# Performance work log

Measured on AMD Instinct MI355X. Metric: run time of the kernel, lower is better.

Reference implementation:

```python
import jax, jax.numpy as jnp
import numpy as np

N = 100000   # nodes
C = 128      # in_channels
K = 32       # n_super_nodes
B = 16       # graphs in batch
TAU = 1.0
EPS = 1e-9
SPARSITY_W = 0.01
TEMPORAL_W = 0.1 * 5
COLLAPSE_W = 2.0


def setup_inputs() -> dict:
    key = jax.random.key(0)
    ks = jax.random.split(key, 8)
    x = jax.random.normal(ks[0], (N, C), dtype=jnp.float32)
    batch = jnp.sort(jax.random.randint(ks[1], (N,), 0, B)).astype(jnp.int64)
    pos = jax.random.normal(ks[2], (N, 2), dtype=jnp.float32)
    gumbel_u = jax.random.uniform(ks[3], (N, K), dtype=jnp.float32,
                                  minval=1e-6, maxval=1.0 - 1e-6)
    W1 = jax.random.normal(ks[4], (C, C), dtype=jnp.float32) / np.float32(np.sqrt(C))
    b1 = jnp.zeros((C,), jnp.float32)
    W2 = jax.random.normal(ks[5], (C, K), dtype=jnp.float32) / np.float32(np.sqrt(C))
    b2 = jnp.zeros((K,), jnp.float32)
    scaling = jnp.asarray(10.0, jnp.float32)
    active_mask = jnp.ones((K,), jnp.float32)
    return dict(x=x, batch=batch, pos=pos, gumbel_u=gumbel_u,
                W1=W1, b1=b1, W2=W2, b2=b2, scaling=scaling,
                active_mask=active_mask)


def reference(x, batch, pos, gumbel_u, W1, b1, W2, b2, scaling, active_mask):
    # assign MLP: Linear -> ReLU -> Linear, scaled
    h = jax.nn.relu(x @ W1 + b1)                      # [N, C]
    logits = (h @ W2 + b2) * scaling                  # [N, K]
    # eval-mode masking of inactive super-nodes (active_mask is a detached buffer)
    mask = jax.lax.stop_gradient(active_mask)[None, :]
    logits = jnp.where(mask == 0, -1e9, logits)
    # Gumbel-softmax (soft, hard=False) with explicit uniform noise
    g = -jnp.log(-jnp.log(gumbel_u + EPS) + EPS)
    s = jax.nn.softmax((logits + g) / TAU, axis=-1)   # [N, K]

    avg_s = s.mean(axis=0)                            # [K]
    entropy = -jnp.mean(jnp.sum(s * jnp.log(s + EPS), axis=1))
    uniform_p = 1.0 / K
    diversity = jnp.sum(uniform_p * jnp.log(uniform_p / (avg_s + EPS)))
    pruning = jnp.mean(jnp.abs(avg_s * (1.0 - active_mask)))
    sparsity = (jnp.sum(active_mask) / K) * SPARSITY_W
    temporal = jnp.asarray(0.0, s.dtype)  # prev_assignments=None

    # collapse prevention (common_losses approximation: normalized entropy
    # deficit + peak-mass penalty), scaled by collapse weight
    ent_avg = -jnp.sum(avg_s * jnp.log(avg_s + EPS))
    collapse = ((jnp.log(jnp.asarray(K, s.dtype)) - ent_avg)
                / jnp.log(jnp.asarray(K, s.dtype))
                + jax.nn.relu(jnp.max(avg_s) - 2.0 / K)) * COLLAPSE_W
    # balance (KL(avg_s || uniform))
    balance = jnp.sum(avg_s * jnp.log(avg_s * K + EPS))

    # spatial variance loss over column-normalized assignments
    s_sum = s.sum(axis=0, keepdims=True) + EPS        # [1, K]
    s_norm = s / s_sum                                # [N, K]
    mu = s_norm.T @ pos                               # [K, 2]
    pos_sq = jnp.sum(pos ** 2, axis=1, keepdims=True) # [N, 1]
    st_pos = s_norm.T @ pos                           # [K, 2]
    var = (s_norm.T @ pos_sq)[:, 0] - 2.0 * jnp.sum(mu * st_pos, axis=1) \
          + jnp.sum(mu ** 2, axis=1)
    spatial = var.mean()

    # per-graph super-node centroids via segment pooling
    sum_s_pos = jax.ops.segment_sum(pos[:, None, :] * s[:, :, None], batch,
                                    num_segments=B)   # [B, K, 2]
    sum_s = jax.ops.segment_sum(s, batch, num_segments=B)[:, :, None] + EPS
    super_node_mu = sum_s_pos / sum_s                 # [B, K, 2]

    # separation loss among centroids
    d = super_node_mu[:, :, None, :] - super_node_mu[:, None, :, :]
    dist_sq = jnp.sum(d ** 2, axis=-1)                # [B, K, K]
    eye = jnp.eye(K, dtype=s.dtype)[None]
    repulsion = 1.0 / (dist_sq + 1.0)
    separation = jnp.sum(repulsion * (1.0 - eye)) / (K * (K - 1) + EPS)

    # hierarchical pooling: out[b,k,c] = sum_{i in graph b} s[i,k] * x[i,c]
    x_expanded = x[:, None, :] * s[:, :, None]        # [N, K, C]
    out = jax.ops.segment_sum(x_expanded, batch, num_segments=B)  # [B, K, C]

    losses = jnp.stack([entropy, diversity, spatial, pruning, sparsity,
                        temporal * TEMPORAL_W, collapse, balance, separation])
    return out, s, super_node_mu, losses
```

## Files before the change

### kernel.cpp

```cpp
#include <hip/hip_runtime.h>
#include <math.h>

#define NN 100000
#define CC 128
#define KK 32
#define BG 16
#define EPSF 1e-9f

#define NTILES 1563

#define S_OFF 65536
#define MU_OFF 3265536
#define LOSS_OFF 3266560

#define WS_ENTARR 0
#define WS_STAT 2048
#define WS_FIRST 4096
#define WS_LAST 4112
#define WS_ZERO_FLOATS 4096

#define W1B_OFF_BYTES 16896
#define W2B_OFF_BYTES 49664
#define WS_PART_FLOAT 16384
#define WS_NEEDED_BYTES (65536ull + (unsigned long long)NTILES * 4096ull * 4ull)

typedef __attribute__((ext_vector_type(8))) _Float16 half8;
typedef __attribute__((ext_vector_type(4))) _Float16 half4v;
typedef __attribute__((ext_vector_type(4))) float float4v;

#define MFMAH(a, b, c) __builtin_amdgcn_mfma_f32_16x16x32_f16((a), (b), (c), 0, 0, 0)

__global__ __launch_bounds__(256) void k_prep(const float* __restrict__ W1,
                                              const float* __restrict__ W2,
                                              _Float16* __restrict__ wW1,
                                              _Float16* __restrict__ wW2,
                                              int* __restrict__ firstp,
                                              int* __restrict__ lastp) {
    int tid = blockIdx.x * 256 + threadIdx.x;
    if (tid < 8 * 4 * 64) {
        int l = tid & 63, ks = (tid >> 6) & 3, nt = tid >> 8;
        int n = nt * 16 + (l & 15);
        int cb = ks * 32 + (l >> 4) * 8;
        half8 H;
#pragma unroll
        for (int j = 0; j < 8; ++j) H[j] = (_Float16)W1[(size_t)(cb + j) * CC + n];
        ((half8*)wW1)[(nt * 4 + ks) * 64 + l] = H;
    } else if (tid < 2048 + 512) {
        int t2 = tid - 2048;
        int l = t2 & 63, ks = (t2 >> 6) & 3, nt = t2 >> 8;
        int n = nt * 16 + (l & 15);
        int cb = ks * 32 + (l >> 4) * 8;
        half8 H;
#pragma unroll
        for (int j = 0; j < 8; ++j) H[j] = (_Float16)W2[(size_t)(cb + j) * KK + n];
        ((half8*)wW2)[(nt * 4 + ks) * 64 + l] = H;
    } else if (tid < 2560 + 16) {
        firstp[tid - 2560] = 0x7fffffff;
    } else if (tid < 2576 + 16) {
        lastp[tid - 2576] = -1;
    }
}

__global__ __launch_bounds__(256, 4) void k_assign(
    const float* __restrict__ x, const int* __restrict__ batch,
    const float* __restrict__ pos, const float* __restrict__ gum,
    const float* __restrict__ b1, const float* __restrict__ b2,
    const float* __restrict__ scaling, const float* __restrict__ amask,
    const _Float16* __restrict__ wW1, const _Float16* __restrict__ wW2,
    float* __restrict__ dout, float* __restrict__ ws,
    float* __restrict__ part, int* __restrict__ firstp, int* __restrict__ lastp)
{
    __shared__ _Float16 xh[64][136];
    __shared__ _Float16 st[32][72];
    __shared__ float lpx[64], lpy[64], lpsq[64];
    __shared__ int lbat[64];
    float* sbuf = (float*)&xh[0][0];

    const int t = threadIdx.x;
    const bool usep = (part != nullptr);
    const int orig = blockIdx.x;
    const int qq = NTILES >> 3, rr8 = NTILES & 7;
    const int xcd = orig & 7, sidx = orig >> 3;
    const int tile = (xcd < rr8 ? xcd * (qq + 1) : rr8 * (qq + 1) + (xcd - rr8) * qq) + sidx;
    const int n0 = tile * 64;

    const int l = t & 63;
    const int wv = __builtin_amdgcn_readfirstlane(t >> 6);
    const int li = l & 15;
    const int g16 = l >> 4;
    const int cc4 = (t & 31) * 4;
    const int nb = t >> 5;
    const int ca  = (2 * wv) * 16 + li;
    const int cb2 = (2 * wv + 1) * 16 + li;
    const int sk = t & 31, sch = t >> 5;

    const float scal = scaling[0];
    const float b2v0 = b2[li], b2v1 = b2[16 + li];
    const float am0 = amask[li], am1 = amask[16 + li];
    const float bv0 = b1[(2 * wv) * 16 + li];
    const float bv1 = b1[(2 * wv + 1) * 16 + li];

#pragma unroll
    for (int r = 0; r < 8; ++r) {
        int n = r * 8 + nb;
        int gn = n0 + n;
        float4 v = make_float4(0.f, 0.f, 0.f, 0.f);
        if (gn < NN) v = *(const float4*)(x + (size_t)gn * CC + cc4);
        *(half4v*)&xh[n][cc4] =
            (half4v){(_Float16)v.x, (_Float16)v.y, (_Float16)v.z, (_Float16)v.w};
    }
    if (t < 64) {
        int gn = n0 + t;
        float px = 0.f, py = 0.f; int bb = BG - 1;
        if (gn < NN) { px = pos[gn * 2]; py = pos[gn * 2 + 1]; bb = batch[gn]; }
        lpx[t] = px; lpy[t] = py; lpsq[t] = px * px + py * py; lbat[t] = bb;
    }

    float gu[8];
#pragma unroll
    for (int r2 = 0; r2 < 4; ++r2) {
        int gn = n0 + wv * 16 + g16 * 4 + r2;
        bool valid = gn < NN;
        gu[r2 * 2]     = valid ? gum[(size_t)gn * KK + li]      : 0.5f;
        gu[r2 * 2 + 1] = valid ? gum[(size_t)gn * KK + 16 + li] : 0.5f;
    }
    __syncthreads();

    half8 vx00, vx01, vx10, vx11;
#pragma unroll
    for (int j = 0; j < 8; ++j) {
        vx00[j] = xh[     g16 * 8 + j][ca];
        vx01[j] = xh[     g16 * 8 + j][cb2];
        vx10[j] = xh[32 + g16 * 8 + j][ca];
        vx11[j] = xh[32 + g16 * 8 + j][cb2];
    }

    float4v acc[4][2];
#pragma unroll
    for (int mt = 0; mt < 4; ++mt) {
        acc[mt][0] = (float4v){0.f, 0.f, 0.f, 0.f};
        acc[mt][1] = (float4v){0.f, 0.f, 0.f, 0.f};
    }
    const half8* W1B = (const half8*)wW1;
#pragma unroll
    for (int ks = 0; ks < 4; ++ks) {
        half8 bh0 = W1B[((2 * wv    ) * 4 + ks) * 64 + l];
        half8 bh1 = W1B[((2 * wv + 1) * 4 + ks) * 64 + l];
#pragma unroll
        for (int mt = 0; mt < 4; ++mt) {
            half8 ah = *(const half8*)&xh[mt * 16 + li][ks * 32 + g16 * 8];
            acc[mt][0] = MFMAH(ah, bh0, acc[mt][0]);
            acc[mt][1] = MFMAH(ah, bh1, acc[mt][1]);
        }
    }
    __syncthreads();

#pragma unroll
    for (int mt = 0; mt < 4; ++mt) {
#pragma unroll
        for (int r2 = 0; r2 < 4; ++r2) {
            int row = mt * 16 + g16 * 4 + r2;
            xh[row][(2 * wv) * 16 + li]     = (_Float16)fmaxf(acc[mt][0][r2] + bv0, 0.f);
            xh[row][(2 * wv + 1) * 16 + li] = (_Float16)fmaxf(acc[mt][1][r2] + bv1, 0.f);
        }
    }
    __syncthreads();

    float4v acc2[2];
    acc2[0] = (float4v){0.f, 0.f, 0.f, 0.f};
    acc2[1] = (float4v){0.f, 0.f, 0.f, 0.f};
    const half8* W2B = (const half8*)wW2;
#pragma unroll
    for (int ks = 0; ks < 4; ++ks) {
        half8 ah = *(const half8*)&xh[wv * 16 + li][ks * 32 + g16 * 8];
        acc2[0] = MFMAH(ah, W2B[(0 * 4 + ks) * 64 + l], acc2[0]);
        acc2[1] = MFMAH(ah, W2B[(1 * 4 + ks) * 64 + l], acc2[1]);
    }

    float ep_acc = 0.f;
#pragma unroll
    for (int r2 = 0; r2 < 4; ++r2) {
        int m = wv * 16 + g16 * 4 + r2;
        int gn = n0 + m;
        bool valid = gn < NN;
        float lg0 = (acc2[0][r2] + b2v0) * scal; if (am0 == 0.f) lg0 = -1e9f;
        float lg1 = (acc2[1][r2] + b2v1) * scal; if (am1 == 0.f) lg1 = -1e9f;
        float z0 = lg0 - __logf(-__logf(gu[r2 * 2] + EPSF) + EPSF);
        float z1 = lg1 - __logf(-__logf(gu[r2 * 2 + 1] + EPSF) + EPSF);
        float e0 = __expf(z0), e1 = __expf(z1);
        float sm = e0 + e1;
        sm += __shfl_xor(sm, 1);
        sm += __shfl_xor(sm, 2);
        sm += __shfl_xor(sm, 4);
        sm += __shfl_xor(sm, 8);
        float inv = 1.f / sm;
        float s0 = e0 * inv, s1 = e1 * inv;
        if (!valid) { s0 = 0.f; s1 = 0.f; }
        else {
            dout[S_OFF + (size_t)gn * KK + li] = s0;
            dout[S_OFF + (size_t)gn * KK + 16 + li] = s1;
        }
        st[li][m] = (_Float16)s0;
        st[16 + li][m] = (_Float16)s1;
        ep_acc += s0 * __logf(s0 + EPSF) + s1 * __logf(s1 + EPSF);
    }
    __syncthreads();

    ep_acc += __shfl_xor(ep_acc, 1);
    ep_acc += __shfl_xor(ep_acc, 2);
    ep_acc += __shfl_xor(ep_acc, 4);
    ep_acc += __shfl_xor(ep_acc, 8);
    ep_acc += __shfl_xor(ep_acc, 16);
    ep_acc += __shfl_xor(ep_acc, 32);
    if (l == 0) sbuf[1024 + wv] = ep_acc;

    const int b0 = lbat[0], b63 = lbat[63];
    int cut = 64;
    if (b0 != b63) {
        for (int i = 1; i < 64; ++i) { if (lbat[i] != b0) { cut = i; break; } }
    }
    const int nseg = (b0 == b63) ? 1 : 2;

#pragma unroll 1
    for (int sg = 0; sg < nseg; ++sg) {
        const int lo = sg ? cut : 0;
        const int hi = sg ? 64 : cut;
        const int bb = sg ? b63 : b0;
        float prs = 0.f, ppx = 0.f, ppy = 0.f, psq = 0.f;
#pragma unroll
        for (int r = 0; r < 8; ++r) {
            int n = sch * 8 + r;
            if (n >= lo && n < hi) {
                float sv = (float)st[sk][n];
                prs += sv; ppx += sv * lpx[n]; ppy += sv * lpy[n]; psq += sv * lpsq[n];
            }
        }
        if (sg) __syncthreads();
        sbuf[(0 * 8 + sch) * 32 + sk] = prs;
        sbuf[(1 * 8 + sch) * 32 + sk] = ppx;
        sbuf[(2 * 8 + sch) * 32 + sk] = ppy;
        sbuf[(3 * 8 + sch) * 32 + sk] = psq;
        __syncthreads();
        if (t < 128) {
            int stat = t >> 5, k = t & 31;
            float a = 0.f;
#pragma unroll
            for (int c = 0; c < 8; ++c) a += sbuf[(stat * 8 + c) * 32 + k];
            atomicAdd(ws + WS_STAT + stat * 512 + bb * KK + k, a);
        }
    }

    if (t == 0) {
        ws[WS_ENTARR + orig] = sbuf[1024] + sbuf[1025] + sbuf[1026] + sbuf[1027];
    }

    float4v p00 = {0.f, 0.f, 0.f, 0.f}, p01 = p00, p10 = p00, p11 = p00;
    auto pool_flush = [&](int bb) {
        float* ob = dout + (size_t)bb * KK * CC;
#pragma unroll
        for (int r2 = 0; r2 < 4; ++r2) {
            int k0r = g16 * 4 + r2;
            atomicAdd(ob + k0r * CC + ca, p00[r2]);
            atomicAdd(ob + k0r * CC + cb2, p01[r2]);
            atomicAdd(ob + (16 + k0r) * CC + ca, p10[r2]);
            atomicAdd(ob + (16 + k0r) * CC + cb2, p11[r2]);
        }
        p00 = (float4v){0.f, 0.f, 0.f, 0.f}; p01 = p00; p10 = p00; p11 = p00;
    };
    if (b0 == b63) {
#pragma unroll
        for (int ksl = 0; ksl < 2; ++ksl) {
            half8 a0 = *(const half8*)&st[li][ksl * 32 + g16 * 8];
            half8 a1 = *(const half8*)&st[16 + li][ksl * 32 + g16 * 8];
            half8 v0 = ksl ? vx10 : vx00;
            half8 v1 = ksl ? vx11 : vx01;
            p00 = MFMAH(a0, v0, p00);
            p01 = MFMAH(a0, v1, p01);
            p10 = MFMAH(a1, v0, p10);
            p11 = MFMAH(a1, v1, p11);
        }
        if (usep) {
            float* pb = part + (size_t)tile * 4096;
#pragma unroll
            for (int r2 = 0; r2 < 4; ++r2) {
                int k0r = g16 * 4 + r2;
                pb[k0r * CC + ca]         = p00[r2];
                pb[k0r * CC + cb2]        = p01[r2];
                pb[(16 + k0r) * CC + ca]  = p10[r2];
                pb[(16 + k0r) * CC + cb2] = p11[r2];
            }
            if (t == 0) {
                atomicMin(firstp + b0, tile);
                atomicMax(lastp + b0, tile);
            }
        } else {
            pool_flush(b0);
        }
    } else {
#pragma unroll 1
        for (int pass = 0; pass < 2; ++pass) {
            int lo = pass ? cut : 0;
            int hi = pass ? 64 : cut;
            int bb = pass ? b63 : b0;
#pragma unroll
            for (int ksl = 0; ksl < 2; ++ksl) {
                half8 a0, a1;
#pragma unroll
                for (int j = 0; j < 8; ++j) {
                    int i = ksl * 32 + g16 * 8 + j;
                    bool in = (i >= lo) && (i < hi);
                    a0[j] = in ? st[li][i] : (_Float16)0.f;
                    a1[j] = in ? st[16 + li][i] : (_Float16)0.f;
                }
                half8 v0 = ksl ? vx10 : vx00;
                half8 v1 = ksl ? vx11 : vx01;
                p00 = MFMAH(a0, v0, p00);
                p01 = MFMAH(a0, v1, p01);
                p10 = MFMAH(a1, v0, p10);
                p11 = MFMAH(a1, v1, p11);
            }
            pool_flush(bb);
        }
    }
}

__global__ __launch_bounds__(256) void k_reduce(const float* __restrict__ part,
                                                const int* __restrict__ firstp,
                                                const int* __restrict__ lastp,
                                                float* __restrict__ dout) {
    const int b   = blockIdx.x >> 7;
    const int elc = (blockIdx.x >> 3) & 15;
    const int sp  = blockIdx.x & 7;
    const int el  = elc * 256 + threadIdx.x;
    const int lo = firstp[b], hi = lastp[b];
    if (lo > hi) return;
    const int count = hi - lo + 1;
    const int per = (count + 7) >> 3;
    const int t0 = lo + sp * per;
    if (t0 > hi) return;
    int t1 = t0 + per - 1; if (t1 > hi) t1 = hi;
    float s0 = 0.f, s1 = 0.f;
    int tt = t0;
    for (; tt + 1 <= t1; tt += 2) {
        s0 += part[(size_t)tt * 4096 + el];
        s1 += part[(size_t)(tt + 1) * 4096 + el];
    }
    if (tt <= t1) s0 += part[(size_t)tt * 4096 + el];
    atomicAdd(dout + (size_t)b * 4096 + el, s0 + s1);
}

__global__ __launch_bounds__(256) void k_final(
    const float* __restrict__ ws, const float* __restrict__ amask,
    float* __restrict__ dout)
{
    __shared__ float avg[32], csum[32], cpx[32], cpy[32], csq[32];
    __shared__ float lmu[16][32][2];
    __shared__ float red[4], ered[4];
    const int t = threadIdx.x;

    float esum = 0.f;
    for (int i = t; i < NTILES; i += 256) esum += ws[WS_ENTARR + i];
    esum += __shfl_xor(esum, 1);
    esum += __shfl_xor(esum, 2);
    esum += __shfl_xor(esum, 4);
    esum += __shfl_xor(esum, 8);
    esum += __shfl_xor(esum, 16);
    esum += __shfl_xor(esum, 32);
    if ((t & 63) == 0) ered[t >> 6] = esum;

    if (t < 32) {
        float a = 0.f, px = 0.f, py = 0.f, sq = 0.f;
        for (int b = 0; b < BG; ++b) {
            a  += ws[WS_STAT + 0 * 512 + b * KK + t];
            px += ws[WS_STAT + 1 * 512 + b * KK + t];
            py += ws[WS_STAT + 2 * 512 + b * KK + t];
            sq += ws[WS_STAT + 3 * 512 + b * KK + t];
        }
        csum[t] = a; cpx[t] = px; cpy[t] = py; csq[t] = sq;
        avg[t] = a / (float)NN;
    }
    for (int idx = t; idx < BG * KK; idx += 256) {
        float den = ws[WS_STAT + idx] + EPSF;
        float mx = ws[WS_STAT + 512 + idx] / den;
        float my = ws[WS_STAT + 1024 + idx] / den;
        int b = idx >> 5, k = idx & 31;
        lmu[b][k][0] = mx; lmu[b][k][1] = my;
        dout[MU_OFF + idx * 2] = mx;
        dout[MU_OFF + idx * 2 + 1] = my;
    }
    __syncthreads();
    float sep = 0.f;
    for (int idx = t; idx < BG * KK * KK; idx += 256) {
        int b = idx >> 10, k1 = (idx >> 5) & 31, k2 = idx & 31;
        if (k1 != k2) {
            float dx = lmu[b][k1][0] - lmu[b][k2][0];
            float dy = lmu[b][k1][1] - lmu[b][k2][1];
            sep += 1.f / (dx * dx + dy * dy + 1.f);
        }
    }
    for (int off = 32; off; off >>= 1) sep += __shfl_down(sep, off);
    if ((t & 63) == 0) red[t >> 6] = sep;
    __syncthreads();
    if (t == 0) {
        float sept = red[0] + red[1] + red[2] + red[3];
        float separation = sept / ((float)(KK * (KK - 1)) + EPSF);
        float entropy = -(ered[0] + ered[1] + ered[2] + ered[3]) / (float)NN;
        float diversity = 0.f, pruning = 0.f, msum = 0.f, entavg = 0.f, bal = 0.f, mxa = 0.f, spatial = 0.f;
        const float up = 1.f / (float)KK;
        for (int k = 0; k < KK; ++k) {
            float a = avg[k];
            diversity += up * logf(up / (a + EPSF));
            float mk = amask[k];
            pruning += fabsf(a * (1.f - mk));
            msum += mk;
            entavg -= a * logf(a + EPSF);
            bal += a * logf(a * (float)KK + EPSF);
            mxa = fmaxf(mxa, a);
            float den = csum[k] + EPSF;
            float mux = cpx[k] / den, muy = cpy[k] / den;
            spatial += csq[k] / den - (mux * mux + muy * muy);
        }
        pruning *= up;
        spatial *= up;
        const float lk = logf((float)KK);
        float collapse = ((lk - entavg) / lk + fmaxf(mxa - 2.f / (float)KK, 0.f)) * 2.0f;
        float sparsity = (msum / (float)KK) * 0.01f;
        dout[LOSS_OFF + 0] = entropy;
        dout[LOSS_OFF + 1] = diversity;
        dout[LOSS_OFF + 2] = spatial;
        dout[LOSS_OFF + 3] = pruning;
        dout[LOSS_OFF + 4] = sparsity;
        dout[LOSS_OFF + 5] = 0.f;
        dout[LOSS_OFF + 6] = collapse;
        dout[LOSS_OFF + 7] = bal;
        dout[LOSS_OFF + 8] = separation;
    }
}

extern "C" void kernel_launch(void* const* d_in, const int* in_sizes, int n_in,
                              void* d_out, int out_size, void* d_ws, size_t ws_size,
                              hipStream_t stream) {
    const float* x     = (const float*)d_in[0];
    const int*   batch = (const int*)d_in[1];
    const float* pos   = (const float*)d_in[2];
    const float* gum   = (const float*)d_in[3];
    const float* W1    = (const float*)d_in[4];
    const float* b1    = (const float*)d_in[5];
    const float* W2    = (const float*)d_in[6];
    const float* b2    = (const float*)d_in[7];
    const float* scal  = (const float*)d_in[8];
    const float* amask = (const float*)d_in[9];
    float* dout = (float*)d_out;
    float* ws   = (float*)d_ws;
    _Float16* wW1 = (_Float16*)((char*)d_ws + W1B_OFF_BYTES);
    _Float16* wW2 = (_Float16*)((char*)d_ws + W2B_OFF_BYTES);
    int* firstp = (int*)(ws + WS_FIRST);
    int* lastp  = (int*)(ws + WS_LAST);
    const bool usep = (ws_size >= (size_t)WS_NEEDED_BYTES);
    float* partp = usep ? (ws + WS_PART_FLOAT) : nullptr;

    hipMemsetAsync(dout, 0, S_OFF * sizeof(float), stream);
    hipMemsetAsync(ws, 0, WS_ZERO_FLOATS * sizeof(float), stream);

    k_prep<<<11, 256, 0, stream>>>(W1, W2, wW1, wW2, firstp, lastp);
    k_assign<<<NTILES, 256, 0, stream>>>(x, batch, pos, gum, b1, b2,
                                         scal, amask, wW1, wW2, dout, ws,
                                         partp, firstp, lastp);
    if (usep) k_reduce<<<BG * 16 * 8, 256, 0, stream>>>(partp, firstp, lastp, dout);
    k_final<<<1, 256, 0, stream>>>(ws, amask, dout);
}
```

Baseline: 83.92 us.

## Store per-tile pooling partials in fp16 and defer s output stores

The per-tile pooling partial sums written to workspace and read back by the reduction kernel are now stored as fp16 instead of fp32, which halves that intermediate traffic and the workspace requirement. The softmax output stores are moved to the end of the assign kernel, keeping values in registers so the stores overlap with the pooling work. The occupancy hint is raised from 4 to 5 blocks per SM. Rounding each partial of up to 64 weighted x values to fp16 loses precision and risks overflow.

```diff
diff --git a/kernel.cpp b/kernel.cpp
--- a/kernel.cpp
+++ b/kernel.cpp
@@ -21,8 +21,8 @@
 
 #define W1B_OFF_BYTES 16896
 #define W2B_OFF_BYTES 49664
-#define WS_PART_FLOAT 16384
-#define WS_NEEDED_BYTES (65536ull + (unsigned long long)NTILES * 4096ull * 4ull)
+#define WS_PART_BYTE 65536
+#define WS_NEEDED_BYTES (65536ull + (unsigned long long)NTILES * 4096ull * 2ull)
 
 typedef __attribute__((ext_vector_type(8))) _Float16 half8;
 typedef __attribute__((ext_vector_type(4))) _Float16 half4v;
@@ -61,14 +61,14 @@
     }
 }
 
-__global__ __launch_bounds__(256, 4) void k_assign(
+__global__ __launch_bounds__(256, 5) void k_assign(
     const float* __restrict__ x, const int* __restrict__ batch,
     const float* __restrict__ pos, const float* __restrict__ gum,
     const float* __restrict__ b1, const float* __restrict__ b2,
     const float* __restrict__ scaling, const float* __restrict__ amask,
     const _Float16* __restrict__ wW1, const _Float16* __restrict__ wW2,
     float* __restrict__ dout, float* __restrict__ ws,
-    float* __restrict__ part, int* __restrict__ firstp, int* __restrict__ lastp)
+    _Float16* __restrict__ part, int* __restrict__ firstp, int* __restrict__ lastp)
 {
     __shared__ _Float16 xh[64][136];
     __shared__ _Float16 st[32][72];
@@ -178,6 +178,7 @@
     }
 
     float ep_acc = 0.f;
+    float sr0[4], sr1[4];
 #pragma unroll
     for (int r2 = 0; r2 < 4; ++r2) {
         int m = wv * 16 + g16 * 4 + r2;
@@ -196,10 +197,7 @@
         float inv = 1.f / sm;
         float s0 = e0 * inv, s1 = e1 * inv;
         if (!valid) { s0 = 0.f; s1 = 0.f; }
-        else {
-            dout[S_OFF + (size_t)gn * KK + li] = s0;
-            dout[S_OFF + (size_t)gn * KK + 16 + li] = s1;
-        }
+        sr0[r2] = s0; sr1[r2] = s1;
         st[li][m] = (_Float16)s0;
         st[16 + li][m] = (_Float16)s1;
         ep_acc += s0 * __logf(s0 + EPSF) + s1 * __logf(s1 + EPSF);
@@ -280,14 +278,14 @@
             p11 = MFMAH(a1, v1, p11);
         }
         if (usep) {
-            float* pb = part + (size_t)tile * 4096;
+            _Float16* pb = part + (size_t)tile * 4096;
 #pragma unroll
             for (int r2 = 0; r2 < 4; ++r2) {
                 int k0r = g16 * 4 + r2;
-                pb[k0r * CC + ca]         = p00[r2];
-                pb[k0r * CC + cb2]        = p01[r2];
-                pb[(16 + k0r) * CC + ca]  = p10[r2];
-                pb[(16 + k0r) * CC + cb2] = p11[r2];
+                pb[k0r * CC + ca]         = (_Float16)p00[r2];
+                pb[k0r * CC + cb2]        = (_Float16)p01[r2];
+                pb[(16 + k0r) * CC + ca]  = (_Float16)p10[r2];
+                pb[(16 + k0r) * CC + cb2] = (_Float16)p11[r2];
             }
             if (t == 0) {
                 atomicMin(firstp + b0, tile);
@@ -322,9 +320,18 @@
             pool_flush(bb);
         }
     }
+
+#pragma unroll
+    for (int r2 = 0; r2 < 4; ++r2) {
+        int gn = n0 + wv * 16 + g16 * 4 + r2;
+        if (gn < NN) {
+            dout[S_OFF + (size_t)gn * KK + li]      = sr0[r2];
+            dout[S_OFF + (size_t)gn * KK + 16 + li] = sr1[r2];
+        }
+    }
 }
 
-__global__ __launch_bounds__(256) void k_reduce(const float* __restrict__ part,
+__global__ __launch_bounds__(256) void k_reduce(const _Float16* __restrict__ part,
                                                 const int* __restrict__ firstp,
                                                 const int* __restrict__ lastp,
                                                 float* __restrict__ dout) {
@@ -342,10 +349,10 @@
     float s0 = 0.f, s1 = 0.f;
     int tt = t0;
     for (; tt + 1 <= t1; tt += 2) {
-        s0 += part[(size_t)tt * 4096 + el];
-        s1 += part[(size_t)(tt + 1) * 4096 + el];
-    }
-    if (tt <= t1) s0 += part[(size_t)tt * 4096 + el];
+        s0 += (float)part[(size_t)tt * 4096 + el];
+        s1 += (float)part[(size_t)(tt + 1) * 4096 + el];
+    }
+    if (tt <= t1) s0 += (float)part[(size_t)tt * 4096 + el];
     atomicAdd(dout + (size_t)b * 4096 + el, s0 + s1);
 }
 
@@ -457,7 +464,7 @@
     int* firstp = (int*)(ws + WS_FIRST);
     int* lastp  = (int*)(ws + WS_LAST);
     const bool usep = (ws_size >= (size_t)WS_NEEDED_BYTES);
-    float* partp = usep ? (ws + WS_PART_FLOAT) : nullptr;
+    _Float16* partp = usep ? (_Float16*)((char*)d_ws + WS_PART_BYTE) : nullptr;
 
     hipMemsetAsync(dout, 0, S_OFF * sizeof(float), stream);
     hipMemsetAsync(ws, 0, WS_ZERO_FLOATS * sizeof(float), stream);
```

Measured after the change: 89.80 us. 7.0% more time.
